# Performance work log

Hardware: AMD Instinct MI355X
Metric: run time of the kernel (lower is better)

## Reference

```python
import jax, jax.numpy as jnp
import numpy as np

N, C, H, E = 4096, 512, 8, 131072
D = C // H
ALPHA = 0.5
EPS = 1e-5


def layer_norm(x, g, b):
    mu = jnp.mean(x, axis=-1, keepdims=True)
    var = jnp.mean((x - mu) ** 2, axis=-1, keepdims=True)
    return (x - mu) * jax.lax.rsqrt(var + EPS) * g + b


def setup_inputs() -> dict:
    key = jax.random.key(0)
    ks = jax.random.split(key, 20)
    s = 0.02
    return {
        "x": jax.random.normal(ks[0], (N, C), jnp.float32),
        "edge_index": jax.random.randint(ks[1], (2, E), 0, N, jnp.int32),
        "local_w": jax.random.normal(ks[2], (C, C), jnp.float32) * s,
        "local_b": jnp.zeros((C,), jnp.float32),
        "in_proj_w": jax.random.normal(ks[3], (3 * C, C), jnp.float32) * s,
        "in_proj_b": jnp.zeros((3 * C,), jnp.float32),
        "attn_out_w": jax.random.normal(ks[4], (C, C), jnp.float32) * s,
        "attn_out_b": jnp.zeros((C,), jnp.float32),
        "output_w": jax.random.normal(ks[5], (C, C), jnp.float32) * s,
        "output_b": jnp.zeros((C,), jnp.float32),
        "norm1_g": jnp.ones((C,), jnp.float32),
        "norm1_b": jnp.zeros((C,), jnp.float32),
        "norm2_g": jnp.ones((C,), jnp.float32),
        "norm2_b": jnp.zeros((C,), jnp.float32),
        "ffn_w1": jax.random.normal(ks[6], (2 * C, C), jnp.float32) * s,
        "ffn_b1": jnp.zeros((2 * C,), jnp.float32),
        "ffn_w2": jax.random.normal(ks[7], (C, 2 * C), jnp.float32) * s,
        "ffn_b2": jnp.zeros((C,), jnp.float32),
    }


def reference(x, edge_index, local_w, local_b, in_proj_w, in_proj_b,
              attn_out_w, attn_out_b, output_w, output_b,
              norm1_g, norm1_b, norm2_g, norm2_b,
              ffn_w1, ffn_b1, ffn_w2, ffn_b2):
    src, dst = edge_index[0], edge_index[1]

    # local branch: linear then scatter-mean over incoming edges
    local_h = x @ local_w.T + local_b                       # [N,C]
    summed = jax.ops.segment_sum(local_h[src], dst, num_segments=N)
    cnt = jax.ops.segment_sum(jnp.ones((E,), x.dtype), dst, num_segments=N)
    local_out = summed / jnp.maximum(cnt, 1.0)[:, None]

    # global branch: full self-attention over all nodes
    qkv = x @ in_proj_w.T + in_proj_b                       # [N,3C]
    q, k, v = jnp.split(qkv, 3, axis=-1)
    q = q.reshape(N, H, D)
    k = k.reshape(N, H, D)
    v = v.reshape(N, H, D)
    scores = jnp.einsum('nhd,mhd->hnm', q, k) / jnp.sqrt(jnp.asarray(D, x.dtype))
    attn = jax.nn.softmax(scores, axis=-1)                  # [H,N,N]
    ctx = jnp.einsum('hnm,mhd->nhd', attn, v).reshape(N, C)
    global_out = ctx @ attn_out_w.T + attn_out_b

    mixed = ALPHA * local_out + (1.0 - ALPHA) * global_out
    hidden = layer_norm(x + (mixed @ output_w.T + output_b), norm1_g, norm1_b)

    ff = jax.nn.gelu(hidden @ ffn_w1.T + ffn_b1, approximate=False) @ ffn_w2.T + ffn_b2
    return layer_norm(hidden + ff, norm2_g, norm2_b)
```

## Files before the change

### kernel.cpp

```cpp
#include <hip/hip_runtime.h>


#define N_NODES 4096
#define C_DIM   512
#define H_HEADS 8
#define D_HEAD  64
#define E_EDGES 131072

typedef unsigned short u16;
typedef unsigned int   u32;
typedef u16   u16x8  __attribute__((ext_vector_type(8)));
typedef __bf16 bf16x8 __attribute__((ext_vector_type(8)));
typedef float  f32x4  __attribute__((ext_vector_type(4)));
typedef u32    u32x4  __attribute__((ext_vector_type(4)));

__device__ __forceinline__ float b2f(u16 u) {
  unsigned int i = ((unsigned int)u) << 16;
  return __builtin_bit_cast(float, i);
}
__device__ __forceinline__ u16 f2b(float f) {
  unsigned int i = __builtin_bit_cast(unsigned int, f);
  i += 0x7fffu + ((i >> 16) & 1u);
  return (u16)(i >> 16);
}
__device__ __forceinline__ u32 cvtpk(float lo, float hi) {
  u32 r;
  asm("v_cvt_pk_bf16_f32 %0, %1, %2" : "=v"(r) : "v"(lo), "v"(hi));
  return r;
}
__device__ __forceinline__ void pl32swap(u32& x, u32& y) {
  asm("v_permlane32_swap_b32 %0, %1" : "+v"(x), "+v"(y));
}
__device__ __forceinline__ void pl16swap(u32& x, u32& y) {
  asm("v_permlane16_swap_b32 %0, %1" : "+v"(x), "+v"(y));
}
__device__ __forceinline__ void glds16(const u16* g, u16* l) {
  __builtin_amdgcn_global_load_lds(
      (const __attribute__((address_space(1))) void*)g,
      (__attribute__((address_space(3))) void*)l, 16, 0, 0);
}

struct CvtArgs {
  const float* src[7];
  u16* dst[7];
  int n[7];
  int* deg;
};

__global__ __launch_bounds__(256) void cvt_multi(CvtArgs a) {
  const int t = blockIdx.y;
  if (t == 7) {
    const int i = blockIdx.x * 256 + threadIdx.x;
    if (i < N_NODES) a.deg[i] = 0;
    return;
  }
  const int i = (blockIdx.x * 256 + threadIdx.x) * 8;
  if (i >= a.n[t]) return;
  const float* s = a.src[t] + i;
  f32x4 v0 = *(const f32x4*)s;
  f32x4 v1 = *(const f32x4*)(s + 4);
  u16x8 o;
  o[0]=f2b(v0[0]); o[1]=f2b(v0[1]); o[2]=f2b(v0[2]); o[3]=f2b(v0[3]);
  o[4]=f2b(v1[0]); o[5]=f2b(v1[1]); o[6]=f2b(v1[2]); o[7]=f2b(v1[3]);
  *(u16x8*)(a.dst[t] + i) = o;
}

template<int EPI>
__global__ __launch_bounds__(256) void gemm_bt(
    const u16* __restrict__ A, const u16* __restrict__ W,
    const float* __restrict__ bias, void* __restrict__ outp,
    int M, int Nout, int K,
    const float* __restrict__ mloc)
{
  const int tid  = threadIdx.x;
  const int lane = tid & 63, wave = tid >> 6;
  const int quad = lane >> 4, l16 = lane & 15;
  const int wm = wave >> 1, wn = wave & 1;
  const int bm = blockIdx.x, bnb = blockIdx.y;

  __shared__ __align__(16) u16 As[64][128];
  __shared__ __align__(16) u16 Ws[64][128];

  f32x4 acc[2][2] = {};

  const int lr4 = lane >> 4, gs = lane & 15;
  const int g8e = (gs ^ lr4) * 8;
  const int g8o = (gs ^ (4 + lr4)) * 8;
  const u16* aw[8];
#pragma unroll
  for (int c = 0; c < 4; ++c) {
    const int g8 = (c & 1) ? g8o : g8e;
    aw[c]     = A + (size_t)(bm  * 64 + wave * 16 + c * 4 + lr4) * K + g8;
    aw[4 + c] = W + (size_t)(bnb * 64 + wave * 16 + c * 4 + lr4) * K + g8;
  }

  for (int k0 = 0; k0 < K; k0 += 128) {
    __syncthreads();
#pragma unroll
    for (int c = 0; c < 4; ++c) {
      glds16(aw[c] + k0,     &As[wave * 16 + c * 4][0]);
      glds16(aw[4 + c] + k0, &Ws[wave * 16 + c * 4][0]);
    }
    __syncthreads();
#pragma unroll
    for (int ks = 0; ks < 4; ++ks) {
      const int slot = ((ks * 4 + quad) ^ (l16 & 7)) * 8;
      bf16x8 af[2], bf[2];
      af[0] = *(const bf16x8*)&As[wm * 32 +      l16][slot];
      af[1] = *(const bf16x8*)&As[wm * 32 + 16 + l16][slot];
      bf[0] = *(const bf16x8*)&Ws[wn * 32 +      l16][slot];
      bf[1] = *(const bf16x8*)&Ws[wn * 32 + 16 + l16][slot];
#pragma unroll
      for (int i = 0; i < 2; ++i)
#pragma unroll
        for (int j = 0; j < 2; ++j)
          acc[i][j] = __builtin_amdgcn_mfma_f32_16x16x32_bf16(af[i], bf[j], acc[i][j], 0, 0, 0);
    }
  }

#pragma unroll
  for (int i = 0; i < 2; ++i)
#pragma unroll
    for (int j = 0; j < 2; ++j) {
      const int col = bnb * 64 + wn * 32 + j * 16 + l16;
      const float bias_v = bias[col];
#pragma unroll
      for (int r = 0; r < 4; ++r) {
        const int row = bm * 64 + wm * 32 + i * 16 + quad * 4 + r;
        float v = acc[i][j][r] + bias_v;
        const size_t o = (size_t)row * Nout + col;
        if constexpr (EPI == 1) {
          ((float*)outp)[o] = v;
        } else if constexpr (EPI == 2) {
          float gl = 0.5f * v * (1.0f + erff(v * 0.70710678118654752f));
          ((u16*)outp)[o] = f2b(gl);
        } else {
          ((u16*)outp)[o] = f2b(0.5f * mloc[o] + 0.5f * v);
        }
      }
    }
}

__global__ __launch_bounds__(256) void gemm128(
    const u16* __restrict__ A, const u16* __restrict__ W,
    const float* __restrict__ bias0, const float* __restrict__ bias1,
    u16* __restrict__ out0, u16* __restrict__ out1,
    int M, int Nout, int K,
    const int* __restrict__ ei, int* __restrict__ deg)
{
  const int tid  = threadIdx.x;
  if (blockIdx.y == 16) {
#pragma unroll
    for (int i = 0; i < 16; ++i) {
      const int e = blockIdx.x * 4096 + i * 256 + tid;
      atomicAdd(&deg[ei[E_EDGES + e]], 1);
    }
    return;
  }
  const int lane = tid & 63, wave = tid >> 6;
  const int quad = lane >> 4, l16 = lane & 15;
  const int wm = wave >> 1, wn = wave & 1;
  const int bm = blockIdx.x, bnb = blockIdx.y;

  __shared__ __align__(16) u16 As[128][64];
  __shared__ __align__(16) u16 Ws[128][64];

  f32x4 acc[4][4] = {};

  const int lr = lane >> 3, gs = lane & 7;
  const int g8 = (gs ^ lr) * 8;
  const u16* ab = A + (size_t)(bm  * 128 + wave * 32 + lr) * K + g8;
  const u16* wb = W + (size_t)(bnb * 128 + wave * 32 + lr) * K + g8;

  for (int k0 = 0; k0 < K; k0 += 64) {
    __syncthreads();
#pragma unroll
    for (int c = 0; c < 4; ++c) {
      glds16(ab + (size_t)(c * 8) * K + k0, &As[wave * 32 + c * 8][0]);
      glds16(wb + (size_t)(c * 8) * K + k0, &Ws[wave * 32 + c * 8][0]);
    }
    __syncthreads();
#pragma unroll
    for (int ks = 0; ks < 2; ++ks) {
      const int slot = ((ks * 4 + quad) ^ (l16 & 7)) * 8;
      bf16x8 af[4], bf[4];
#pragma unroll
      for (int am = 0; am < 4; ++am)
        af[am] = *(const bf16x8*)&As[wm * 64 + am * 16 + l16][slot];
#pragma unroll
      for (int bn = 0; bn < 4; ++bn)
        bf[bn] = *(const bf16x8*)&Ws[wn * 64 + bn * 16 + l16][slot];
#pragma unroll
      for (int am = 0; am < 4; ++am)
#pragma unroll
        for (int bn = 0; bn < 4; ++bn)
          acc[am][bn] = __builtin_amdgcn_mfma_f32_16x16x32_bf16(af[am], bf[bn], acc[am][bn], 0, 0, 0);
    }
  }

#pragma unroll
  for (int am = 0; am < 4; ++am)
#pragma unroll
    for (int bn = 0; bn < 4; ++bn) {
      const int col = bnb * 128 + wn * 64 + bn * 16 + l16;
      const float bias_v = (col < 512) ? bias0[col] : bias1[col - 512];
#pragma unroll
      for (int r = 0; r < 4; ++r) {
        const int row = bm * 128 + wm * 64 + am * 16 + quad * 4 + r;
        float v = acc[am][bn][r] + bias_v;
        if (col < 512) out0[(size_t)row * 512 + col] = f2b(v);
        else           out1[(size_t)row * 1536 + (col - 512)] = f2b(v);
      }
    }
}

__global__ __launch_bounds__(256) void scan_vtrans(
    const int* __restrict__ deg, int* __restrict__ off, int* __restrict__ cursor,
    const u16* __restrict__ qkv, u16* __restrict__ vt)
{
  if (blockIdx.x == 512) {
    __shared__ int part[256];
    const int t = threadIdx.x;
    int v[16];
    int s = 0;
#pragma unroll
    for (int i = 0; i < 16; ++i) { v[i] = deg[t * 16 + i]; s += v[i]; }
    part[t] = s;
    __syncthreads();
    for (int d = 1; d < 256; d <<= 1) {
      int val = (t >= d) ? part[t - d] : 0;
      __syncthreads();
      if (t >= d) part[t] += val;
      __syncthreads();
    }
    int prefix = (t == 0) ? 0 : part[t - 1];
#pragma unroll
    for (int i = 0; i < 16; ++i) {
      off[t * 16 + i] = prefix;
      cursor[t * 16 + i] = prefix;
      prefix += v[i];
    }
    if (t == 255) off[4096] = prefix;
    return;
  }
  __shared__ __align__(16) u16 T[64][64];
  const int tid = threadIdx.x;
  const int h = blockIdx.x >> 6, mt = blockIdx.x & 63;
  const int m0 = mt * 64;
  const int c  = tid & 7;
  const int mr = tid >> 3;
#pragma unroll
  for (int half = 0; half < 2; ++half) {
    const int m = mr + half * 32;
    const u16x8 v = *(const u16x8*)(qkv + (size_t)(m0 + m) * 1536 + 1024 + h * 64 + c * 8);
    *(u16x8*)&T[m][((c ^ (m >> 3)) * 8)] = v;
  }
  __syncthreads();
#pragma unroll
  for (int half = 0; half < 2; ++half) {
    const int q = tid + half * 256;
    const int d = q >> 3, mc = q & 7;
    u16x8 w;
#pragma unroll
    for (int e = 0; e < 8; ++e)
      w[e] = T[mc * 8 + e][(((d >> 3) ^ mc) * 8) + (d & 7)];
    *(u16x8*)(vt + (size_t)(h * 64 + d) * N_NODES + m0 + mc * 8) = w;
  }
}

template<int SPLITS>
__global__ __launch_bounds__(256) void attn_kernel(
    const u16* __restrict__ qkv, const u16* __restrict__ vt,
    u16* __restrict__ opart, float* __restrict__ lpart,
    const int* __restrict__ ei, int* __restrict__ cursor, int* __restrict__ csr)
{
  const int tid = threadIdx.x, wave = tid >> 6, lane = tid & 63;
  const int split = blockIdx.z;
  if (split == SPLITS) {
    const int sblk = blockIdx.y * 32 + blockIdx.x;
#pragma unroll
    for (int i = 0; i < 2; ++i) {
      const int e = sblk * 512 + i * 256 + tid;
      const int s = ei[e];
      const int d = ei[E_EDGES + e];
      const int p = atomicAdd(&cursor[d], 1);
      csr[p] = s;
    }
    return;
  }
  const int quad = lane >> 4, l16 = lane & 15;
  const int h = blockIdx.x & 7;
  const int tile = (blockIdx.x >> 3) + (blockIdx.y << 2);

  __shared__ __align__(16) u16 Ks[2][64][64];
  __shared__ __align__(16) u16 Vts[2][64][64];

  const float QSCALE = 0.18033688011112042f;
  bf16x8 aq[2][2];
#pragma unroll
  for (int mb = 0; mb < 2; ++mb) {
    const int qrow = tile * 128 + wave * 32 + mb * 16 + l16;
    const u16* qp = qkv + (size_t)qrow * 1536 + h * 64 + quad * 8;
    u16x8 q0 = *(const u16x8*)qp;
    u16x8 q1 = *(const u16x8*)(qp + 32);
    u16x8 s0, s1;
#pragma unroll
    for (int i = 0; i < 8; ++i) {
      s0[i] = f2b(b2f(q0[i]) * QSCALE);
      s1[i] = f2b(b2f(q1[i]) * QSCALE);
    }
    aq[mb][0] = __builtin_bit_cast(bf16x8, s0);
    aq[mb][1] = __builtin_bit_cast(bf16x8, s1);
  }

  f32x4 O[2][4] = {};
  float lsum[2] = {};

  const int lr = lane >> 3, gs = lane & 7;
  const int g8 = (gs ^ lr) * 8;
  const int R0 = wave * 16 + lr;

  const u16* kp = qkv + (size_t)R0 * 1536 + 512 + h * 64 + g8;
  const u16* vp = vt + (size_t)(h * 64 + R0) * N_NODES + g8;

  const int mt0 = split * (64 / SPLITS), mt1 = (split + 1) * (64 / SPLITS);

  {
    const size_t ko = (size_t)mt0 * 64 * 1536;
    glds16(kp + ko,            &Ks[0][wave * 16][0]);
    glds16(kp + ko + 8 * 1536, &Ks[0][wave * 16 + 8][0]);
    glds16(vp + mt0 * 64,               &Vts[0][wave * 16][0]);
    glds16(vp + mt0 * 64 + 8 * N_NODES, &Vts[0][wave * 16 + 8][0]);
  }

  for (int mt = mt0; mt < mt1; ++mt) {
    const int cur = (mt - mt0) & 1;
    if (mt + 1 < mt1) {
      const size_t ko = (size_t)(mt + 1) * 64 * 1536;
      glds16(kp + ko,            &Ks[cur ^ 1][wave * 16][0]);
      glds16(kp + ko + 8 * 1536, &Ks[cur ^ 1][wave * 16 + 8][0]);
      glds16(vp + (mt + 1) * 64,               &Vts[cur ^ 1][wave * 16][0]);
      glds16(vp + (mt + 1) * 64 + 8 * N_NODES, &Vts[cur ^ 1][wave * 16 + 8][0]);
      asm volatile("s_waitcnt vmcnt(4)" ::: "memory");
    } else {
      asm volatile("s_waitcnt vmcnt(0)" ::: "memory");
    }
    __builtin_amdgcn_s_barrier();
    __builtin_amdgcn_sched_barrier(0);

    f32x4 st[2][4] = {};
    __builtin_amdgcn_s_setprio(1);
#pragma unroll
    for (int ks = 0; ks < 2; ++ks) {
      const int slot = ((ks * 4 + quad) ^ (l16 & 7)) * 8;
      bf16x8 af[4];
#pragma unroll
      for (int jn = 0; jn < 4; ++jn)
        af[jn] = *(const bf16x8*)&Ks[cur][jn * 16 + l16][slot];
#pragma unroll
      for (int mb = 0; mb < 2; ++mb)
#pragma unroll
        for (int jn = 0; jn < 4; ++jn)
          st[mb][jn] = __builtin_amdgcn_mfma_f32_16x16x32_bf16(af[jn], aq[mb][ks], st[mb][jn], 0, 0, 0);
    }
    __builtin_amdgcn_s_setprio(0);

    bf16x8 pa[2][2];
#pragma unroll
    for (int mb = 0; mb < 2; ++mb) {
      u32 pk[4][2];
#pragma unroll
      for (int jn = 0; jn < 4; ++jn) {
        float p0 = __builtin_amdgcn_exp2f(st[mb][jn][0]);
        float p1 = __builtin_amdgcn_exp2f(st[mb][jn][1]);
        float p2 = __builtin_amdgcn_exp2f(st[mb][jn][2]);
        float p3 = __builtin_amdgcn_exp2f(st[mb][jn][3]);
        lsum[mb] += (p0 + p1) + (p2 + p3);
        pk[jn][0] = cvtpk(p0, p1);
        pk[jn][1] = cvtpk(p2, p3);
      }
#pragma unroll
      for (int ks = 0; ks < 2; ++ks) {
        u32 x0 = pk[2 * ks][0], y0 = pk[2 * ks + 1][0];
        u32 x1 = pk[2 * ks][1], y1 = pk[2 * ks + 1][1];
        pl32swap(x0, y0); pl16swap(x0, y0);
        pl32swap(x1, y1); pl16swap(x1, y1);
        u32x4 av;
        av[0] = x0; av[1] = x1; av[2] = y0; av[3] = y1;
        pa[mb][ks] = __builtin_bit_cast(bf16x8, av);
      }
    }

    __builtin_amdgcn_s_setprio(1);
#pragma unroll
    for (int ks = 0; ks < 2; ++ks) {
      const int slot = ((ks * 4 + quad) ^ (l16 & 7)) * 8;
      bf16x8 bv[4];
#pragma unroll
      for (int jd = 0; jd < 4; ++jd)
        bv[jd] = *(const bf16x8*)&Vts[cur][jd * 16 + l16][slot];
#pragma unroll
      for (int mb = 0; mb < 2; ++mb)
#pragma unroll
        for (int jd = 0; jd < 4; ++jd)
          O[mb][jd] = __builtin_amdgcn_mfma_f32_16x16x32_bf16(pa[mb][ks], bv[jd], O[mb][jd], 0, 0, 0);
    }
    __builtin_amdgcn_s_setprio(0);
    __builtin_amdgcn_s_barrier();
  }

#pragma unroll
  for (int mb = 0; mb < 2; ++mb) {
    float ls = lsum[mb];
    ls += __shfl_xor(ls, 16);
    ls += __shfl_xor(ls, 32);
#pragma unroll
    for (int r = 0; r < 4; ++r) {
      const int row = tile * 128 + wave * 32 + mb * 16 + quad * 4 + r;
      u16* orow = opart + ((size_t)split * N_NODES + row) * C_DIM + h * 64;
#pragma unroll
      for (int jd = 0; jd < 4; ++jd)
        orow[jd * 16 + l16] = f2b(O[mb][jd][r]);
    }
    if (lane < 16) {
      const int row = tile * 128 + wave * 32 + mb * 16 + l16;
      lpart[((size_t)split * N_NODES + row) * H_HEADS + h] = ls;
    }
  }
}

template<int SPLITS>
__global__ __launch_bounds__(256) void combine_gather(
    const u16* __restrict__ opart, const float* __restrict__ lpart,
    u16* __restrict__ ctx,
    const int* __restrict__ off, const int* __restrict__ csr,
    const u16* __restrict__ lh, float* __restrict__ lo)
{
  if (blockIdx.y == 0) {
    const int wave = threadIdx.x >> 6, lane = threadIdx.x & 63;
    const int n = blockIdx.x * 4 + wave;
    const int j0 = off[n], j1 = off[n + 1];
    float acc[8] = {};
    int j = j0;
    for (; j + 4 <= j1; j += 4) {
      const int s0 = csr[j], s1 = csr[j + 1], s2 = csr[j + 2], s3 = csr[j + 3];
      const u16x8 v0 = *(const u16x8*)(lh + (size_t)s0 * C_DIM + lane * 8);
      const u16x8 v1 = *(const u16x8*)(lh + (size_t)s1 * C_DIM + lane * 8);
      const u16x8 v2 = *(const u16x8*)(lh + (size_t)s2 * C_DIM + lane * 8);
      const u16x8 v3 = *(const u16x8*)(lh + (size_t)s3 * C_DIM + lane * 8);
#pragma unroll
      for (int i = 0; i < 8; ++i)
        acc[i] += (b2f(v0[i]) + b2f(v1[i])) + (b2f(v2[i]) + b2f(v3[i]));
    }
    for (; j < j1; ++j) {
      const int s = csr[j];
      const u16x8 v = *(const u16x8*)(lh + (size_t)s * C_DIM + lane * 8);
#pragma unroll
      for (int i = 0; i < 8; ++i) acc[i] += b2f(v[i]);
    }
    const float inv = 1.0f / fmaxf((float)(j1 - j0), 1.0f);
    f32x4 o0, o1;
#pragma unroll
    for (int i = 0; i < 4; ++i) { o0[i] = acc[i] * inv; o1[i] = acc[4 + i] * inv; }
    float* op = lo + (size_t)n * C_DIM + lane * 8;
    *(f32x4*)op = o0;
    *(f32x4*)(op + 4) = o1;
    return;
  }
  const size_t base = (size_t)(blockIdx.x * 256 + threadIdx.x) * 8;
  const int row = (int)(base >> 9);
  const int h = (int)((base & 511) >> 6);
  float l = 0.0f;
#pragma unroll
  for (int s = 0; s < SPLITS; ++s)
    l += lpart[(size_t)s * N_NODES * H_HEADS + (size_t)row * H_HEADS + h];
  const float inv = 1.0f / l;
  float o[8] = {};
#pragma unroll
  for (int s = 0; s < SPLITS; ++s) {
    const u16x8 p = *(const u16x8*)(opart + (size_t)s * N_NODES * C_DIM + base);
#pragma unroll
    for (int i = 0; i < 8; ++i) o[i] += b2f(p[i]);
  }
  u16x8 ob;
#pragma unroll
  for (int i = 0; i < 8; ++i) ob[i] = f2b(o[i] * inv);
  *(u16x8*)(ctx + base) = ob;
}

__global__ __launch_bounds__(256) void ln1_kernel(
    const float* __restrict__ x, const float* __restrict__ pr,
    const float* __restrict__ g, const float* __restrict__ b,
    u16* __restrict__ hb, float* __restrict__ hf)
{
  const int wave = threadIdx.x >> 6, lane = threadIdx.x & 63;
  const int row = blockIdx.x * 4 + wave;
  const int c0 = lane * 8;
  const size_t base = (size_t)row * C_DIM + c0;
  f32x4 x0 = *(const f32x4*)(x + base);
  f32x4 x1 = *(const f32x4*)(x + base + 4);
  f32x4 p0 = *(const f32x4*)(pr + base);
  f32x4 p1 = *(const f32x4*)(pr + base + 4);
  float v[8];
#pragma unroll
  for (int i = 0; i < 4; ++i) { v[i] = x0[i] + p0[i]; v[4 + i] = x1[i] + p1[i]; }
  float sum = 0, sq = 0;
#pragma unroll
  for (int i = 0; i < 8; ++i) { sum += v[i]; sq += v[i] * v[i]; }
  for (int off = 1; off < 64; off <<= 1) { sum += __shfl_xor(sum, off); sq += __shfl_xor(sq, off); }
  const float mean = sum * (1.0f / C_DIM);
  const float var  = sq * (1.0f / C_DIM) - mean * mean;
  const float rstd = rsqrtf(var + 1e-5f);
  f32x4 g0 = *(const f32x4*)(g + c0), g1 = *(const f32x4*)(g + c0 + 4);
  f32x4 b0 = *(const f32x4*)(b + c0), b1 = *(const f32x4*)(b + c0 + 4);
  u16x8 ob; f32x4 h0, h1;
#pragma unroll
  for (int i = 0; i < 4; ++i) {
    float hv0 = (v[i]     - mean) * rstd * g0[i] + b0[i];
    float hv1 = (v[4 + i] - mean) * rstd * g1[i] + b1[i];
    h0[i] = hv0; h1[i] = hv1;
    ob[i] = f2b(hv0); ob[4 + i] = f2b(hv1);
  }
  *(u16x8*)(hb + base) = ob;
  *(f32x4*)(hf + base) = h0;
  *(f32x4*)(hf + base + 4) = h1;
}

__global__ __launch_bounds__(256) void ln2_kernel(
    const float* __restrict__ a, const float* __restrict__ c,
    const float* __restrict__ g, const float* __restrict__ b,
    float* __restrict__ out)
{
  const int wave = threadIdx.x >> 6, lane = threadIdx.x & 63;
  const int row = blockIdx.x * 4 + wave;
  const int c0 = lane * 8;
  const size_t base = (size_t)row * C_DIM + c0;
  f32x4 a0 = *(const f32x4*)(a + base), a1 = *(const f32x4*)(a + base + 4);
  f32x4 c0v = *(const f32x4*)(c + base), c1v = *(const f32x4*)(c + base + 4);
  float v[8];
#pragma unroll
  for (int i = 0; i < 4; ++i) { v[i] = a0[i] + c0v[i]; v[4 + i] = a1[i] + c1v[i]; }
  float sum = 0, sq = 0;
#pragma unroll
  for (int i = 0; i < 8; ++i) { sum += v[i]; sq += v[i] * v[i]; }
  for (int off = 1; off < 64; off <<= 1) { sum += __shfl_xor(sum, off); sq += __shfl_xor(sq, off); }
  const float mean = sum * (1.0f / C_DIM);
  const float var  = sq * (1.0f / C_DIM) - mean * mean;
  const float rstd = rsqrtf(var + 1e-5f);
  f32x4 g0 = *(const f32x4*)(g + c0), g1 = *(const f32x4*)(g + c0 + 4);
  f32x4 b0 = *(const f32x4*)(b + c0), b1 = *(const f32x4*)(b + c0 + 4);
  f32x4 h0, h1;
#pragma unroll
  for (int i = 0; i < 4; ++i) {
    h0[i] = (v[i]     - mean) * rstd * g0[i] + b0[i];
    h1[i] = (v[4 + i] - mean) * rstd * g1[i] + b1[i];
  }
  *(f32x4*)(out + base) = h0;
  *(f32x4*)(out + base + 4) = h1;
}

extern "C" void kernel_launch(void* const* d_in, const int* in_sizes, int n_in,
                              void* d_out, int out_size, void* d_ws, size_t ws_size,
                              hipStream_t stream) {
  const float* x          = (const float*)d_in[0];
  const int*   ei         = (const int*)d_in[1];
  const float* local_w    = (const float*)d_in[2];
  const float* local_b    = (const float*)d_in[3];
  const float* in_proj_w  = (const float*)d_in[4];
  const float* in_proj_b  = (const float*)d_in[5];
  const float* attn_out_w = (const float*)d_in[6];
  const float* attn_out_b = (const float*)d_in[7];
  const float* output_w   = (const float*)d_in[8];
  const float* output_b   = (const float*)d_in[9];
  const float* n1g = (const float*)d_in[10];
  const float* n1b = (const float*)d_in[11];
  const float* n2g = (const float*)d_in[12];
  const float* n2b = (const float*)d_in[13];
  const float* ffn_w1 = (const float*)d_in[14];
  const float* ffn_b1 = (const float*)d_in[15];
  const float* ffn_w2 = (const float*)d_in[16];
  const float* ffn_b2 = (const float*)d_in[17];
  float* out = (float*)d_out;

  char* ws = (char*)d_ws;
  size_t o = 0;
  float* local_out = (float*)(ws + o); o += (size_t)N_NODES * C_DIM * 4;
  int* deg    = (int*)(ws + o); o += (N_NODES) * 4;
  int* off    = (int*)(ws + o); o += (N_NODES + 16) * 4;
  int* cursor = (int*)(ws + o); o += (N_NODES) * 4;
  int* csr    = (int*)(ws + o); o += (size_t)E_EDGES * 4;
  u16* xb   = (u16*)(ws + o); o += (size_t)N_NODES * C_DIM * 2;
  u16* wbLQ = (u16*)(ws + o); o += (size_t)4 * C_DIM * C_DIM * 2;
  u16* wbA  = (u16*)(ws + o); o += (size_t)C_DIM * C_DIM * 2;
  u16* wbO  = (u16*)(ws + o); o += (size_t)C_DIM * C_DIM * 2;
  u16* wbF1 = (u16*)(ws + o); o += (size_t)2 * C_DIM * C_DIM * 2;
  u16* wbF2 = (u16*)(ws + o); o += (size_t)2 * C_DIM * C_DIM * 2;
  u16* local_h   = (u16*)(ws + o); o += (size_t)N_NODES * C_DIM * 2;
  u16* qkvb      = (u16*)(ws + o); o += (size_t)N_NODES * 3 * C_DIM * 2;
  u16* ctxb      = (u16*)(ws + o); o += (size_t)N_NODES * C_DIM * 2;
  u16* mixed     = (u16*)(ws + o); o += (size_t)N_NODES * C_DIM * 2;
  u16* hidden_bf = (u16*)(ws + o); o += (size_t)N_NODES * C_DIM * 2;
  float* hidden_f = (float*)(ws + o); o += (size_t)N_NODES * C_DIM * 4;
  u16* ff1       = (u16*)(ws + o); o += (size_t)N_NODES * 2 * C_DIM * 2;
  float* proj  = (float*)qkvb;
  float* ff2   = (float*)local_out;
  u16*   vt    = xb;
  u16* opart4 = (u16*)(ws + o);
  float* lpart4 = (float*)(ws + o + (size_t)4 * N_NODES * C_DIM * 2);
  const size_t need4 = o + (size_t)4 * N_NODES * C_DIM * 2 + (size_t)4 * N_NODES * H_HEADS * 4;
  const bool use4 = (ws_size >= need4);
  u16* opart2 = (u16*)hidden_bf;
  float* lpart2 = (float*)(opart2 + (size_t)2 * N_NODES * C_DIM);

  CvtArgs ca;
  ca.src[0] = x;          ca.dst[0] = xb;   ca.n[0] = N_NODES * C_DIM;
  ca.src[1] = local_w;    ca.dst[1] = wbLQ;                  ca.n[1] = C_DIM * C_DIM;
  ca.src[2] = in_proj_w;  ca.dst[2] = wbLQ + C_DIM * C_DIM;  ca.n[2] = 3 * C_DIM * C_DIM;
  ca.src[3] = attn_out_w; ca.dst[3] = wbA;  ca.n[3] = C_DIM * C_DIM;
  ca.src[4] = output_w;   ca.dst[4] = wbO;  ca.n[4] = C_DIM * C_DIM;
  ca.src[5] = ffn_w1;     ca.dst[5] = wbF1; ca.n[5] = 2 * C_DIM * C_DIM;
  ca.src[6] = ffn_w2;     ca.dst[6] = wbF2; ca.n[6] = 2 * C_DIM * C_DIM;
  ca.deg = deg;
  cvt_multi<<<dim3(N_NODES * C_DIM / 2048, 8), 256, 0, stream>>>(ca);

  gemm128<<<dim3(32, 17), 256, 0, stream>>>(xb, wbLQ, local_b, in_proj_b,
      local_h, qkvb, N_NODES, 4 * C_DIM, C_DIM, ei, deg);

  scan_vtrans<<<513, 256, 0, stream>>>(deg, off, cursor, qkvb, vt);

  if (use4) {
    attn_kernel<4><<<dim3(32, 8, 5), 256, 0, stream>>>(qkvb, vt, opart4, lpart4,
        ei, cursor, csr);
    combine_gather<4><<<dim3(1024, 2), 256, 0, stream>>>(opart4, lpart4, ctxb,
        off, csr, local_h, local_out);
  } else {
    attn_kernel<2><<<dim3(32, 8, 3), 256, 0, stream>>>(qkvb, vt, opart2, lpart2,
        ei, cursor, csr);
    combine_gather<2><<<dim3(1024, 2), 256, 0, stream>>>(opart2, lpart2, ctxb,
        off, csr, local_h, local_out);
  }

  gemm_bt<3><<<dim3(64, 8), 256, 0, stream>>>(ctxb, wbA, attn_out_b, mixed,
      N_NODES, C_DIM, C_DIM, local_out);

  gemm_bt<1><<<dim3(64, 8), 256, 0, stream>>>(mixed, wbO, output_b, proj,
      N_NODES, C_DIM, C_DIM, nullptr);
  ln1_kernel<<<N_NODES / 4, 256, 0, stream>>>(x, proj, n1g, n1b, hidden_bf, hidden_f);

  gemm_bt<2><<<dim3(64, 16), 256, 0, stream>>>(hidden_bf, wbF1, ffn_b1, ff1,
      N_NODES, 2 * C_DIM, C_DIM, nullptr);
  gemm_bt<1><<<dim3(64, 8), 256, 0, stream>>>(ff1, wbF2, ffn_b2, ff2,
      N_NODES, C_DIM, 2 * C_DIM, nullptr);
  ln2_kernel<<<N_NODES / 4, 256, 0, stream>>>(hidden_f, ff2, n2g, n2b, out);
}
```

Before: 242.8 us.

## Triple-buffer attention K/V loads, compute row sums via MFMA, use 128-tile FFN1 GEMM

The attention kernel moves from double to triple buffering of K/V tiles in shared memory. Each tile's load is issued two iterations ahead, which lets the trailing barrier of every iteration be dropped. The softmax denominator is now accumulated with an extra MFMA against a vector of ones instead of scalar adds and cross-lane shuffles. Separately, the FFN first GEMM with GELU is routed through the 128x128-tile gemm128 kernel via a new template epilogue. Together these aim to hide load latency, cut VALU work and raise data reuse, at the cost of more LDS per block (possibly lower occupancy) and a few more MFMA instructions.

```diff
diff --git a/kernel.cpp b/kernel.cpp
--- a/kernel.cpp
+++ b/kernel.cpp
@@ -141,6 +141,7 @@
     }
 }
 
+template<int EPI>
 __global__ __launch_bounds__(256) void gemm128(
     const u16* __restrict__ A, const u16* __restrict__ W,
     const float* __restrict__ bias0, const float* __restrict__ bias1,
@@ -149,13 +150,15 @@
     const int* __restrict__ ei, int* __restrict__ deg)
 {
   const int tid  = threadIdx.x;
-  if (blockIdx.y == 16) {
-#pragma unroll
-    for (int i = 0; i < 16; ++i) {
-      const int e = blockIdx.x * 4096 + i * 256 + tid;
-      atomicAdd(&deg[ei[E_EDGES + e]], 1);
-    }
-    return;
+  if constexpr (EPI == 0) {
+    if (blockIdx.y == 16) {
+#pragma unroll
+      for (int i = 0; i < 16; ++i) {
+        const int e = blockIdx.x * 4096 + i * 256 + tid;
+        atomicAdd(&deg[ei[E_EDGES + e]], 1);
+      }
+      return;
+    }
   }
   const int lane = tid & 63, wave = tid >> 6;
   const int quad = lane >> 4, l16 = lane & 15;
@@ -203,13 +206,19 @@
 #pragma unroll
     for (int bn = 0; bn < 4; ++bn) {
       const int col = bnb * 128 + wn * 64 + bn * 16 + l16;
-      const float bias_v = (col < 512) ? bias0[col] : bias1[col - 512];
 #pragma unroll
       for (int r = 0; r < 4; ++r) {
         const int row = bm * 128 + wm * 64 + am * 16 + quad * 4 + r;
-        float v = acc[am][bn][r] + bias_v;
-        if (col < 512) out0[(size_t)row * 512 + col] = f2b(v);
-        else           out1[(size_t)row * 1536 + (col - 512)] = f2b(v);
+        if constexpr (EPI == 0) {
+          const float bias_v = (col < 512) ? bias0[col] : bias1[col - 512];
+          float v = acc[am][bn][r] + bias_v;
+          if (col < 512) out0[(size_t)row * 512 + col] = f2b(v);
+          else           out1[(size_t)row * 1536 + (col - 512)] = f2b(v);
+        } else {
+          float v = acc[am][bn][r] + bias0[col];
+          float gl = 0.5f * v * (1.0f + erff(v * 0.70710678118654752f));
+          out0[(size_t)row * Nout + col] = f2b(gl);
+        }
       }
     }
 }
@@ -292,8 +301,8 @@
   const int h = blockIdx.x & 7;
   const int tile = (blockIdx.x >> 3) + (blockIdx.y << 2);
 
-  __shared__ __align__(16) u16 Ks[2][64][64];
-  __shared__ __align__(16) u16 Vts[2][64][64];
+  __shared__ __align__(16) u16 Ks[3][64][64];
+  __shared__ __align__(16) u16 Vts[3][64][64];
 
   const float QSCALE = 0.18033688011112042f;
   bf16x8 aq[2][2];
@@ -313,8 +322,13 @@
     aq[mb][1] = __builtin_bit_cast(bf16x8, s1);
   }
 
+  u16x8 ones_u;
+#pragma unroll
+  for (int i = 0; i < 8; ++i) ones_u[i] = 0x3F80;
+  const bf16x8 vone = __builtin_bit_cast(bf16x8, ones_u);
+
   f32x4 O[2][4] = {};
-  float lsum[2] = {};
+  f32x4 lacc[2] = {};
 
   const int lr = lane >> 3, gs = lane & 7;
   const int g8 = (gs ^ lr) * 8;
@@ -325,28 +339,31 @@
 
   const int mt0 = split * (64 / SPLITS), mt1 = (split + 1) * (64 / SPLITS);
 
-  {
-    const size_t ko = (size_t)mt0 * 64 * 1536;
-    glds16(kp + ko,            &Ks[0][wave * 16][0]);
-    glds16(kp + ko + 8 * 1536, &Ks[0][wave * 16 + 8][0]);
-    glds16(vp + mt0 * 64,               &Vts[0][wave * 16][0]);
-    glds16(vp + mt0 * 64 + 8 * N_NODES, &Vts[0][wave * 16 + 8][0]);
-  }
+#define STAGE(MT, B)                                                      \
+  do {                                                                    \
+    const size_t ko_ = (size_t)(MT) * 64 * 1536;                          \
+    glds16(kp + ko_,            &Ks[(B)][wave * 16][0]);                  \
+    glds16(kp + ko_ + 8 * 1536, &Ks[(B)][wave * 16 + 8][0]);              \
+    glds16(vp + (MT) * 64,               &Vts[(B)][wave * 16][0]);        \
+    glds16(vp + (MT) * 64 + 8 * N_NODES, &Vts[(B)][wave * 16 + 8][0]);    \
+  } while (0)
+
+  STAGE(mt0, 0);
+  STAGE(mt0 + 1, 1);
 
   for (int mt = mt0; mt < mt1; ++mt) {
-    const int cur = (mt - mt0) & 1;
+    const int i = mt - mt0;
+    const int cur = i % 3;
     if (mt + 1 < mt1) {
-      const size_t ko = (size_t)(mt + 1) * 64 * 1536;
-      glds16(kp + ko,            &Ks[cur ^ 1][wave * 16][0]);
-      glds16(kp + ko + 8 * 1536, &Ks[cur ^ 1][wave * 16 + 8][0]);
-      glds16(vp + (mt + 1) * 64,               &Vts[cur ^ 1][wave * 16][0]);
-      glds16(vp + (mt + 1) * 64 + 8 * N_NODES, &Vts[cur ^ 1][wave * 16 + 8][0]);
       asm volatile("s_waitcnt vmcnt(4)" ::: "memory");
     } else {
       asm volatile("s_waitcnt vmcnt(0)" ::: "memory");
     }
     __builtin_amdgcn_s_barrier();
     __builtin_amdgcn_sched_barrier(0);
+    if (mt + 2 < mt1) {
+      STAGE(mt + 2, (i + 2) % 3);
+    }
 
     f32x4 st[2][4] = {};
     __builtin_amdgcn_s_setprio(1);
@@ -375,7 +392,6 @@
         float p1 = __builtin_amdgcn_exp2f(st[mb][jn][1]);
         float p2 = __builtin_amdgcn_exp2f(st[mb][jn][2]);
         float p3 = __builtin_amdgcn_exp2f(st[mb][jn][3]);
-        lsum[mb] += (p0 + p1) + (p2 + p3);
         pk[jn][0] = cvtpk(p0, p1);
         pk[jn][1] = cvtpk(p2, p3);
       }
@@ -400,20 +416,19 @@
       for (int jd = 0; jd < 4; ++jd)
         bv[jd] = *(const bf16x8*)&Vts[cur][jd * 16 + l16][slot];
 #pragma unroll
-      for (int mb = 0; mb < 2; ++mb)
+      for (int mb = 0; mb < 2; ++mb) {
 #pragma unroll
         for (int jd = 0; jd < 4; ++jd)
           O[mb][jd] = __builtin_amdgcn_mfma_f32_16x16x32_bf16(pa[mb][ks], bv[jd], O[mb][jd], 0, 0, 0);
+        lacc[mb] = __builtin_amdgcn_mfma_f32_16x16x32_bf16(pa[mb][ks], vone, lacc[mb], 0, 0, 0);
+      }
     }
     __builtin_amdgcn_s_setprio(0);
-    __builtin_amdgcn_s_barrier();
-  }
+  }
+#undef STAGE
 
 #pragma unroll
   for (int mb = 0; mb < 2; ++mb) {
-    float ls = lsum[mb];
-    ls += __shfl_xor(ls, 16);
-    ls += __shfl_xor(ls, 32);
 #pragma unroll
     for (int r = 0; r < 4; ++r) {
       const int row = tile * 128 + wave * 32 + mb * 16 + quad * 4 + r;
@@ -421,10 +436,8 @@
 #pragma unroll
       for (int jd = 0; jd < 4; ++jd)
         orow[jd * 16 + l16] = f2b(O[mb][jd][r]);
-    }
-    if (lane < 16) {
-      const int row = tile * 128 + wave * 32 + mb * 16 + l16;
-      lpart[((size_t)split * N_NODES + row) * H_HEADS + h] = ls;
+      if (l16 == 0)
+        lpart[((size_t)split * N_NODES + row) * H_HEADS + h] = lacc[mb][r];
     }
   }
 }
@@ -623,7 +636,7 @@
   ca.deg = deg;
   cvt_multi<<<dim3(N_NODES * C_DIM / 2048, 8), 256, 0, stream>>>(ca);
 
-  gemm128<<<dim3(32, 17), 256, 0, stream>>>(xb, wbLQ, local_b, in_proj_b,
+  gemm128<0><<<dim3(32, 17), 256, 0, stream>>>(xb, wbLQ, local_b, in_proj_b,
       local_h, qkvb, N_NODES, 4 * C_DIM, C_DIM, ei, deg);
 
   scan_vtrans<<<513, 256, 0, stream>>>(deg, off, cursor, qkvb, vt);
@@ -647,8 +660,8 @@
       N_NODES, C_DIM, C_DIM, nullptr);
   ln1_kernel<<<N_NODES / 4, 256, 0, stream>>>(x, proj, n1g, n1b, hidden_bf, hidden_f);
 
-  gemm_bt<2><<<dim3(64, 16), 256, 0, stream>>>(hidden_bf, wbF1, ffn_b1, ff1,
-      N_NODES, 2 * C_DIM, C_DIM, nullptr);
+  gemm128<2><<<dim3(32, 8), 256, 0, stream>>>(hidden_bf, wbF1, ffn_b1, nullptr,
+      ff1, nullptr, N_NODES, 2 * C_DIM, C_DIM, nullptr, nullptr);
   gemm_bt<1><<<dim3(64, 8), 256, 0, stream>>>(ff1, wbF2, ffn_b2, ff2,
       N_NODES, C_DIM, 2 * C_DIM, nullptr);
   ln2_kernel<<<N_NODES / 4, 256, 0, stream>>>(hidden_f, ff2, n2g, n2b, out);
```

New measurement: 251.9 us. 3.7% more time.

## Fold attn_out projection into output projection via precomputed fused weight

Applied to the files above, without the earlier changes.

The attention-output GEMM and the output-projection GEMM are merged algebraically. A fused weight Wo·Wa is computed on device, along with a fused bias row 0.5·Wo·ba+bo. The mixed projection then becomes a single K=1024 GEMM over the concatenated [local_out, ctx] inputs. local_out is stored in bf16 instead of fp32, and the FFN1 GELU GEMM moves to the 128-tile kernel. This removes one full N×C GEMM and its intermediate round trip, at the cost of extra weight-prep work folded into existing launches and different bf16 rounding of the fused weights.

```diff
diff --git a/kernel.cpp b/kernel.cpp
--- a/kernel.cpp
+++ b/kernel.cpp
@@ -45,6 +45,8 @@
   u16* dst[7];
   int n[7];
   int* deg;
+  const float* awf;
+  u16* waT;
 };
 
 __global__ __launch_bounds__(256) void cvt_multi(CvtArgs a) {
@@ -52,6 +54,36 @@
   if (t == 7) {
     const int i = blockIdx.x * 256 + threadIdx.x;
     if (i < N_NODES) a.deg[i] = 0;
+    return;
+  }
+  if (t == 8) {
+    if (blockIdx.x >= 64) return;
+    __shared__ __align__(16) u16 T[64][64];
+    const int b = blockIdx.x;
+    const int j0 = (b & 7) * 64, n0 = (b >> 3) * 64;
+    const int c = threadIdx.x & 7, mr = threadIdx.x >> 3;
+#pragma unroll
+    for (int half = 0; half < 2; ++half) {
+      const int j = mr + half * 32;
+      const float* sp = a.awf + (size_t)(j0 + j) * 512 + n0 + c * 8;
+      f32x4 a0 = *(const f32x4*)sp;
+      f32x4 a1 = *(const f32x4*)(sp + 4);
+      u16x8 v;
+#pragma unroll
+      for (int e = 0; e < 4; ++e) { v[e] = f2b(a0[e]); v[4 + e] = f2b(a1[e]); }
+      *(u16x8*)&T[j][((c ^ (j >> 3)) * 8)] = v;
+    }
+    __syncthreads();
+#pragma unroll
+    for (int half = 0; half < 2; ++half) {
+      const int q = threadIdx.x + half * 256;
+      const int n = q >> 3, mc = q & 7;
+      u16x8 w;
+#pragma unroll
+      for (int e = 0; e < 8; ++e)
+        w[e] = T[mc * 8 + e][(((n >> 3) ^ mc) * 8) + (n & 7)];
+      *(u16x8*)(a.waT + (size_t)(n0 + n) * 512 + j0 + mc * 8) = w;
+    }
     return;
   }
   const int i = (blockIdx.x * 256 + threadIdx.x) * 8;
@@ -70,7 +102,7 @@
     const u16* __restrict__ A, const u16* __restrict__ W,
     const float* __restrict__ bias, void* __restrict__ outp,
     int M, int Nout, int K,
-    const float* __restrict__ mloc)
+    const u16* __restrict__ A2, const u16* __restrict__ W2)
 {
   const int tid  = threadIdx.x;
   const int lane = tid & 63, wave = tid >> 6;
@@ -86,20 +118,38 @@
   const int lr4 = lane >> 4, gs = lane & 15;
   const int g8e = (gs ^ lr4) * 8;
   const int g8o = (gs ^ (4 + lr4)) * 8;
+  const int SA = (EPI == 4) ? 512 : K;
   const u16* aw[8];
+  const u16* aw2[8];
 #pragma unroll
   for (int c = 0; c < 4; ++c) {
     const int g8 = (c & 1) ? g8o : g8e;
-    aw[c]     = A + (size_t)(bm  * 64 + wave * 16 + c * 4 + lr4) * K + g8;
-    aw[4 + c] = W + (size_t)(bnb * 64 + wave * 16 + c * 4 + lr4) * K + g8;
+    const int rowA = bm  * 64 + wave * 16 + c * 4 + lr4;
+    const int rowW = bnb * 64 + wave * 16 + c * 4 + lr4;
+    aw[c]     = A + (size_t)rowA * SA + g8;
+    aw[4 + c] = W + (size_t)rowW * SA + g8;
+    if constexpr (EPI == 4) {
+      aw2[c]     = A2 + (size_t)rowA * 512 + g8;
+      aw2[4 + c] = W2 + (size_t)rowW * 512 + g8;
+    }
   }
 
   for (int k0 = 0; k0 < K; k0 += 128) {
     __syncthreads();
-#pragma unroll
-    for (int c = 0; c < 4; ++c) {
-      glds16(aw[c] + k0,     &As[wave * 16 + c * 4][0]);
-      glds16(aw[4 + c] + k0, &Ws[wave * 16 + c * 4][0]);
+    if constexpr (EPI == 4) {
+      const bool lo = (k0 < 512);
+      const int kk = lo ? k0 : k0 - 512;
+#pragma unroll
+      for (int c = 0; c < 4; ++c) {
+        glds16((lo ? aw[c]     : aw2[c])     + kk, &As[wave * 16 + c * 4][0]);
+        glds16((lo ? aw[4 + c] : aw2[4 + c]) + kk, &Ws[wave * 16 + c * 4][0]);
+      }
+    } else {
+#pragma unroll
+      for (int c = 0; c < 4; ++c) {
+        glds16(aw[c] + k0,     &As[wave * 16 + c * 4][0]);
+        glds16(aw[4 + c] + k0, &Ws[wave * 16 + c * 4][0]);
+      }
     }
     __syncthreads();
 #pragma unroll
@@ -127,40 +177,69 @@
 #pragma unroll
       for (int r = 0; r < 4; ++r) {
         const int row = bm * 64 + wm * 32 + i * 16 + quad * 4 + r;
-        float v = acc[i][j][r] + bias_v;
         const size_t o = (size_t)row * Nout + col;
         if constexpr (EPI == 1) {
-          ((float*)outp)[o] = v;
+          ((float*)outp)[o] = acc[i][j][r] + bias_v;
         } else if constexpr (EPI == 2) {
+          float v = acc[i][j][r] + bias_v;
           float gl = 0.5f * v * (1.0f + erff(v * 0.70710678118654752f));
           ((u16*)outp)[o] = f2b(gl);
         } else {
-          ((u16*)outp)[o] = f2b(0.5f * mloc[o] + 0.5f * v);
+          ((float*)outp)[o] = 0.5f * acc[i][j][r] + bias_v;
         }
       }
     }
 }
 
+template<int EPI>
 __global__ __launch_bounds__(256) void gemm128(
     const u16* __restrict__ A, const u16* __restrict__ W,
     const float* __restrict__ bias0, const float* __restrict__ bias1,
     u16* __restrict__ out0, u16* __restrict__ out1,
     int M, int Nout, int K,
-    const int* __restrict__ ei, int* __restrict__ deg)
+    const int* __restrict__ ei, int* __restrict__ deg,
+    const u16* __restrict__ wfA, const u16* __restrict__ waTp,
+    u16* __restrict__ wfB, const float* __restrict__ wo_f32,
+    const float* __restrict__ ba_f32, const float* __restrict__ bo_f32,
+    float* __restrict__ bfrow)
 {
   const int tid  = threadIdx.x;
-  if (blockIdx.y == 16) {
-#pragma unroll
-    for (int i = 0; i < 16; ++i) {
-      const int e = blockIdx.x * 4096 + i * 256 + tid;
-      atomicAdd(&deg[ei[E_EDGES + e]], 1);
-    }
-    return;
+  const u16* Ap = A;
+  const u16* Wp = W;
+  int bm = blockIdx.x, bnb = blockIdx.y;
+  bool wfmode = false;
+  if constexpr (EPI == 0) {
+    if (blockIdx.y == 16) {
+#pragma unroll
+      for (int i = 0; i < 16; ++i) {
+        const int e = blockIdx.x * 4096 + i * 256 + tid;
+        atomicAdd(&deg[ei[E_EDGES + e]], 1);
+      }
+      return;
+    }
+    if (blockIdx.y == 17) {
+      if (blockIdx.x == 16) {
+        for (int dd = tid; dd < 512; dd += 256) {
+          const float* wrow = wo_f32 + (size_t)dd * 512;
+          float s = 0.f;
+          for (int j = 0; j < 512; j += 4) {
+            f32x4 w4 = *(const f32x4*)(wrow + j);
+            f32x4 b4 = *(const f32x4*)(ba_f32 + j);
+            s += (w4[0] * b4[0] + w4[1] * b4[1]) + (w4[2] * b4[2] + w4[3] * b4[3]);
+          }
+          bfrow[dd] = 0.5f * s + bo_f32[dd];
+        }
+        return;
+      }
+      if (blockIdx.x > 16) return;
+      wfmode = true;
+      Ap = wfA; Wp = waTp;
+      bm = blockIdx.x & 3; bnb = blockIdx.x >> 2;
+    }
   }
   const int lane = tid & 63, wave = tid >> 6;
   const int quad = lane >> 4, l16 = lane & 15;
   const int wm = wave >> 1, wn = wave & 1;
-  const int bm = blockIdx.x, bnb = blockIdx.y;
 
   __shared__ __align__(16) u16 As[128][64];
   __shared__ __align__(16) u16 Ws[128][64];
@@ -169,8 +248,8 @@
 
   const int lr = lane >> 3, gs = lane & 7;
   const int g8 = (gs ^ lr) * 8;
-  const u16* ab = A + (size_t)(bm  * 128 + wave * 32 + lr) * K + g8;
-  const u16* wb = W + (size_t)(bnb * 128 + wave * 32 + lr) * K + g8;
+  const u16* ab = Ap + (size_t)(bm  * 128 + wave * 32 + lr) * K + g8;
+  const u16* wb = Wp + (size_t)(bnb * 128 + wave * 32 + lr) * K + g8;
 
   for (int k0 = 0; k0 < K; k0 += 64) {
     __syncthreads();
@@ -203,13 +282,23 @@
 #pragma unroll
     for (int bn = 0; bn < 4; ++bn) {
       const int col = bnb * 128 + wn * 64 + bn * 16 + l16;
-      const float bias_v = (col < 512) ? bias0[col] : bias1[col - 512];
 #pragma unroll
       for (int r = 0; r < 4; ++r) {
         const int row = bm * 128 + wm * 64 + am * 16 + quad * 4 + r;
-        float v = acc[am][bn][r] + bias_v;
-        if (col < 512) out0[(size_t)row * 512 + col] = f2b(v);
-        else           out1[(size_t)row * 1536 + (col - 512)] = f2b(v);
+        if constexpr (EPI == 0) {
+          if (wfmode) {
+            wfB[(size_t)row * 512 + col] = f2b(acc[am][bn][r]);
+          } else {
+            const float bias_v = (col < 512) ? bias0[col] : bias1[col - 512];
+            float v = acc[am][bn][r] + bias_v;
+            if (col < 512) out0[(size_t)row * 512 + col] = f2b(v);
+            else           out1[(size_t)row * 1536 + (col - 512)] = f2b(v);
+          }
+        } else {
+          float v = acc[am][bn][r] + bias0[col];
+          float gl = 0.5f * v * (1.0f + erff(v * 0.70710678118654752f));
+          out0[(size_t)row * Nout + col] = f2b(gl);
+        }
       }
     }
 }
@@ -434,7 +523,7 @@
     const u16* __restrict__ opart, const float* __restrict__ lpart,
     u16* __restrict__ ctx,
     const int* __restrict__ off, const int* __restrict__ csr,
-    const u16* __restrict__ lh, float* __restrict__ lo)
+    const u16* __restrict__ lh, u16* __restrict__ lo)
 {
   if (blockIdx.y == 0) {
     const int wave = threadIdx.x >> 6, lane = threadIdx.x & 63;
@@ -459,12 +548,10 @@
       for (int i = 0; i < 8; ++i) acc[i] += b2f(v[i]);
     }
     const float inv = 1.0f / fmaxf((float)(j1 - j0), 1.0f);
-    f32x4 o0, o1;
-#pragma unroll
-    for (int i = 0; i < 4; ++i) { o0[i] = acc[i] * inv; o1[i] = acc[4 + i] * inv; }
-    float* op = lo + (size_t)n * C_DIM + lane * 8;
-    *(f32x4*)op = o0;
-    *(f32x4*)(op + 4) = o1;
+    u16x8 ob;
+#pragma unroll
+    for (int i = 0; i < 8; ++i) ob[i] = f2b(acc[i] * inv);
+    *(u16x8*)(lo + (size_t)n * C_DIM + lane * 8) = ob;
     return;
   }
   const size_t base = (size_t)(blockIdx.x * 256 + threadIdx.x) * 8;
@@ -605,6 +692,10 @@
   float* proj  = (float*)qkvb;
   float* ff2   = (float*)local_out;
   u16*   vt    = xb;
+  u16*   lo_bf = (u16*)local_out;
+  u16* waT = mixed;
+  u16* wfB = mixed + 262144;
+  float* bf_row = (float*)(mixed + 524288);
   u16* opart4 = (u16*)(ws + o);
   float* lpart4 = (float*)(ws + o + (size_t)4 * N_NODES * C_DIM * 2);
   const size_t need4 = o + (size_t)4 * N_NODES * C_DIM * 2 + (size_t)4 * N_NODES * H_HEADS * 4;
@@ -621,10 +712,13 @@
   ca.src[5] = ffn_w1;     ca.dst[5] = wbF1; ca.n[5] = 2 * C_DIM * C_DIM;
   ca.src[6] = ffn_w2;     ca.dst[6] = wbF2; ca.n[6] = 2 * C_DIM * C_DIM;
   ca.deg = deg;
-  cvt_multi<<<dim3(N_NODES * C_DIM / 2048, 8), 256, 0, stream>>>(ca);
-
-  gemm128<<<dim3(32, 17), 256, 0, stream>>>(xb, wbLQ, local_b, in_proj_b,
-      local_h, qkvb, N_NODES, 4 * C_DIM, C_DIM, ei, deg);
+  ca.awf = attn_out_w;
+  ca.waT = waT;
+  cvt_multi<<<dim3(N_NODES * C_DIM / 2048, 9), 256, 0, stream>>>(ca);
+
+  gemm128<0><<<dim3(32, 18), 256, 0, stream>>>(xb, wbLQ, local_b, in_proj_b,
+      local_h, qkvb, N_NODES, 4 * C_DIM, C_DIM, ei, deg,
+      wbO, waT, wfB, output_w, attn_out_b, output_b, bf_row);
 
   scan_vtrans<<<513, 256, 0, stream>>>(deg, off, cursor, qkvb, vt);
 
@@ -632,24 +726,23 @@
     attn_kernel<4><<<dim3(32, 8, 5), 256, 0, stream>>>(qkvb, vt, opart4, lpart4,
         ei, cursor, csr);
     combine_gather<4><<<dim3(1024, 2), 256, 0, stream>>>(opart4, lpart4, ctxb,
-        off, csr, local_h, local_out);
+        off, csr, local_h, lo_bf);
   } else {
     attn_kernel<2><<<dim3(32, 8, 3), 256, 0, stream>>>(qkvb, vt, opart2, lpart2,
         ei, cursor, csr);
     combine_gather<2><<<dim3(1024, 2), 256, 0, stream>>>(opart2, lpart2, ctxb,
-        off, csr, local_h, local_out);
-  }
-
-  gemm_bt<3><<<dim3(64, 8), 256, 0, stream>>>(ctxb, wbA, attn_out_b, mixed,
-      N_NODES, C_DIM, C_DIM, local_out);
-
-  gemm_bt<1><<<dim3(64, 8), 256, 0, stream>>>(mixed, wbO, output_b, proj,
-      N_NODES, C_DIM, C_DIM, nullptr);
+        off, csr, local_h, lo_bf);
+  }
+
+  gemm_bt<4><<<dim3(64, 8), 256, 0, stream>>>(lo_bf, wbO, bf_row, proj,
+      N_NODES, C_DIM, 2 * C_DIM, ctxb, wfB);
+
   ln1_kernel<<<N_NODES / 4, 256, 0, stream>>>(x, proj, n1g, n1b, hidden_bf, hidden_f);
 
-  gemm_bt<2><<<dim3(64, 16), 256, 0, stream>>>(hidden_bf, wbF1, ffn_b1, ff1,
-      N_NODES, 2 * C_DIM, C_DIM, nullptr);
+  gemm128<2><<<dim3(32, 8), 256, 0, stream>>>(hidden_bf, wbF1, ffn_b1, nullptr,
+      ff1, nullptr, N_NODES, 2 * C_DIM, C_DIM, nullptr, nullptr,
+      nullptr, nullptr, nullptr, nullptr, nullptr, nullptr, nullptr);
   gemm_bt<1><<<dim3(64, 8), 256, 0, stream>>>(ff1, wbF2, ffn_b2, ff2,
-      N_NODES, C_DIM, 2 * C_DIM, nullptr);
+      N_NODES, C_DIM, 2 * C_DIM, nullptr, nullptr);
   ln2_kernel<<<N_NODES / 4, 256, 0, stream>>>(hidden_f, ff2, n2g, n2b, out);
 }
```

After: 279.3 us. +15.0%, slower.
